# Kernel optimization log

Measured on AMD Instinct MI355X. Metric: run time of the kernel, lower is better.

The kernel has to match this reference:

```python
import jax, jax.numpy as jnp
import numpy as np

BS, N, H, W, C3D, K = 2, 4096, 64, 192, 64, 3


def _leaky(x):
    return jnp.where(x >= 0, x, 0.1 * x)


def setup_inputs() -> dict:
    key = jax.random.key(0)
    ks = jax.random.split(key, 10)
    # uv: pixel coordinates (x in [0,W), y in [0,H)), channel-first [bs,2,N]
    uv = jax.random.uniform(ks[0], (BS, 2, N), dtype=jnp.float32)
    uv = uv * jnp.array([W, H], dtype=jnp.float32)[None, :, None]
    feat_2d = jax.random.normal(ks[1], (BS, 64, H, W), dtype=jnp.float32)
    feat_3d = jax.random.normal(ks[2], (BS, C3D, N), dtype=jnp.float32)
    w1 = jax.random.normal(ks[3], (16, 3), dtype=jnp.float32) * 0.3
    b1 = jax.random.normal(ks[4], (16,), dtype=jnp.float32) * 0.1
    w2 = jax.random.normal(ks[5], (C3D, 16), dtype=jnp.float32) * 0.2
    b2 = jax.random.normal(ks[6], (C3D,), dtype=jnp.float32) * 0.1
    w_out = jax.random.normal(ks[7], (C3D, C3D), dtype=jnp.float32) * 0.1
    b_out = jax.random.normal(ks[8], (C3D,), dtype=jnp.float32) * 0.1
    return {"uv": uv, "feat_2d": feat_2d, "feat_3d": feat_3d,
            "w1": w1, "b1": b1, "w2": w2, "b2": b2,
            "w_out": w_out, "b_out": b_out}


def reference(uv, feat_2d, feat_3d, w1, b1, w2, b2, w_out, b_out):
    bs, _, image_h, image_w = feat_2d.shape
    c3d = feat_3d.shape[1]
    hw = image_h * image_w

    # mesh grid, channel order (x, y), flattened row-major over (h, w): [bs,2,HW]
    ys, xs = jnp.meshgrid(jnp.arange(image_h, dtype=jnp.float32),
                          jnp.arange(image_w, dtype=jnp.float32), indexing='ij')
    grid = jnp.stack([xs.ravel(), ys.ravel()], axis=0)  # [2, HW]
    grid = jnp.broadcast_to(grid[None], (bs, 2, hw))

    # k-NN of uv points for each grid query: squared distances [bs, HW, N]
    d2 = (jnp.sum(grid * grid, axis=1)[:, :, None]
          + jnp.sum(uv * uv, axis=1)[:, None, :]
          - 2.0 * jnp.einsum('bcq,bcn->bqn', grid, uv))
    _, knn_idx = jax.lax.top_k(-d2, K)  # [bs, HW, K]

    # gather uv and feat_3d by neighbor indices: [bs, 2+C, HW, K]
    data = jnp.concatenate([uv, feat_3d], axis=1)
    knn = jax.vmap(lambda d, i: d[:, i])(data, knn_idx)
    knn_uv, knn_feat3d = knn[:, :2], knn[:, 2:]

    knn_offset = knn_uv - grid[..., None]                      # [bs,2,HW,K]
    offset_norm = jnp.linalg.norm(knn_offset, axis=1, keepdims=True)
    score_in = jnp.concatenate([knn_offset, offset_norm], 1)   # [bs,3,HW,K]

    # score net: 1x1 conv (3->16, leaky_relu 0.1) -> 1x1 conv (16->C, sigmoid)
    h1 = _leaky(jnp.einsum('bcqk,oc->boqk', score_in, w1) + b1[None, :, None, None])
    score = jax.nn.sigmoid(jnp.einsum('bcqk,oc->boqk', h1, w2) + b2[None, :, None, None])

    final = jnp.sum(score * knn_feat3d, axis=-1)               # [bs,C,HW]
    final = final.reshape(bs, c3d, image_h, image_w)

    # out conv: 1x1 conv (C->C) + leaky_relu 0.1
    out = _leaky(jnp.einsum('bchw,oc->bohw', final, w_out) + b_out[None, :, None, None])
    return out
```

## Files before the change

kernel.cpp:

```cpp
#include <hip/hip_runtime.h>
#include <math.h>

#define NBS 2
#define NPTS 4096
#define HH 64
#define WW 192
#define HW (HH*WW)
#define NC 64
#define GX 48
#define GY 16
#define NCELL (GX*GY)
#define CSB 1024

#define FBIG 3.0e38f
#define IBIG 0x7FFFFFFF

__global__ __launch_bounds__(256) void k0_prep(
    const float* __restrict__ uv, const float* __restrict__ f3d,
    float* __restrict__ f3dT, float4* __restrict__ binned,
    int* __restrict__ cellStart) {
#pragma clang fp contract(off)
  int bid = blockIdx.x;
  int t = threadIdx.x;
  if (bid < 2) {
    int b = bid;
    __shared__ int hist[NCELL];
    __shared__ int cum[NCELL];
    __shared__ int cur[NCELL];
    for (int c = t; c < NCELL; c += 256) hist[c] = 0;
    __syncthreads();
    const float* u0p = uv + (size_t)b * 2 * NPTS;
    const float* u1p = u0p + NPTS;
    for (int n = t; n < NPTS; n += 256) {
      float u0 = u0p[n], u1 = u1p[n];
      int cxp = min((int)(u0 * 0.25f), GX - 1);
      int cyp = min((int)(u1 * 0.25f), GY - 1);
      atomicAdd(&hist[cyp * GX + cxp], 1);
    }
    __syncthreads();
    if (t < 64) {
      int carry = 0;
#pragma unroll
      for (int ck = 0; ck < NCELL / 64; ++ck) {
        int v = hist[ck * 64 + t];
#pragma unroll
        for (int off = 1; off < 64; off <<= 1) {
          int u = __shfl_up(v, off);
          if (t >= off) v += u;
        }
        cum[ck * 64 + t] = v + carry;
        carry += __shfl(v, 63);
      }
    }
    __syncthreads();
    if (t == 0) cellStart[b * CSB] = 0;
    for (int c = t; c < NCELL; c += 256) {
      cellStart[b * CSB + c + 1] = cum[c];
      cur[c] = cum[c] - hist[c];
    }
    __syncthreads();
    for (int n = t; n < NPTS; n += 256) {
      float u0 = u0p[n], u1 = u1p[n];
      float s0 = u0 * u0;
      float s1 = u1 * u1;
      float uu = s0 + s1;
      int cxp = min((int)(u0 * 0.25f), GX - 1);
      int cyp = min((int)(u1 * 0.25f), GY - 1);
      int pos = atomicAdd(&cur[cyp * GX + cxp], 1);
      binned[(size_t)b * NPTS + pos] =
          make_float4(u0 + u0, u1 + u1, uu, __int_as_float(n));
    }
  } else {
    int bb = bid - 2;
    int b = bb >> 7;
    int half = (bb >> 6) & 1;
    int nt = (bb & 63) << 6;
    __shared__ float tile[32][65];
    int n_in = t & 63;
    int r0 = t >> 6;
    const float* src = f3d + (size_t)b * NC * NPTS + (size_t)half * 32 * NPTS;
#pragma unroll
    for (int r = 0; r < 8; ++r) {
      int c = r0 + (r << 2);
      tile[c][n_in] = src[(size_t)c * NPTS + nt + n_in];
    }
    __syncthreads();
    float* dst = f3dT + ((size_t)b * NPTS + nt) * NC + half * 32;
    int c_out = t & 31;
    int n0 = t >> 5;
#pragma unroll
    for (int r = 0; r < 8; ++r) {
      int n = n0 + (r << 3);
      dst[(size_t)n * NC + c_out] = tile[c_out][n];
    }
  }
}

__global__ __launch_bounds__(256) void k_main(
    const float4* __restrict__ binned, const int* __restrict__ cellStart,
    const float* __restrict__ uv, const float* __restrict__ f3dT,
    const float* __restrict__ w1, const float* __restrict__ b1,
    const float* __restrict__ w2, const float* __restrict__ b2,
    const float* __restrict__ w_out, const float* __restrict__ b_out,
    float* __restrict__ out) {
#pragma clang fp contract(off)
  int t = threadIdx.x;
  int b = blockIdx.y;

  __shared__ int sidx[16][4];
  __shared__ float sh1f[16 * 52];
  __shared__ float fin[16][68];

  {
    int Q = t >> 4;
    int j = t & 15;
    int qi = blockIdx.x * 16 + Q;
    int x = qi % WW, y = qi / WW;
    float xf = (float)x, yf = (float)y;
    float gg = xf * xf + yf * yf;
    int cx = x >> 2, cy = y >> 2;

    const float4* __restrict__ pts = binned + (size_t)b * NPTS;
    const int* __restrict__ cs = cellStart + b * CSB;

    float v0 = FBIG, v1 = FBIG, v2 = FBIG;
    int i0 = IBIG, i1 = IBIG, i2 = IBIG;

    auto ins = [&](float d, int gi) {
      bool dup = (gi == i0) || (gi == i1) || (gi == i2);
      bool lt2 = !dup && ((d < v2) || (d == v2 && gi < i2));
      bool lt1 = !dup && ((d < v1) || (d == v1 && gi < i1));
      bool lt0 = !dup && ((d < v0) || (d == v0 && gi < i0));
      i2 = lt1 ? i1 : (lt2 ? gi : i2);
      v2 = lt1 ? v1 : (lt2 ? d : v2);
      i1 = lt0 ? i0 : (lt1 ? gi : i1);
      v1 = lt0 ? v0 : (lt1 ? d : v1);
      i0 = lt0 ? gi : i0;
      v0 = lt0 ? d : v0;
    };
    auto scanRow = [&](int ry, int cA, int cB) {
      int s = cs[ry * GX + cA];
      int e = cs[ry * GX + cB + 1];
      for (int n = s + j; n < e; n += 16) {
        float4 p = pts[n];
        float d = (gg + p.z) - __builtin_fmaf(yf, p.y, xf * p.x);
        ins(d, __float_as_int(p.w));
      }
    };
    auto mergeAll = [&]() {
#pragma unroll
      for (int m = 1; m <= 8; m <<= 1) {
        float ov0 = __shfl_xor(v0, m), ov1 = __shfl_xor(v1, m),
              ov2 = __shfl_xor(v2, m);
        int oi0 = __shfl_xor(i0, m), oi1 = __shfl_xor(i1, m),
            oi2 = __shfl_xor(i2, m);
        ins(ov0, oi0); ins(ov1, oi1); ins(ov2, oi2);
      }
    };

    int cxL = max(cx - 1, 0), cxH = min(cx + 1, GX - 1);
    int cyL = max(cy - 1, 0), cyH = min(cy + 1, GY - 1);
    for (int ry = cyL; ry <= cyH; ++ry) scanRow(ry, cxL, cxH);
    mergeAll();

    while (true) {
      bool fullDom = (cxL == 0 && cxH == GX - 1 && cyL == 0 && cyH == GY - 1);
      float dL = (cxL > 0) ? (xf - (float)(cxL * 4)) : FBIG;
      float dR = (cxH < GX - 1) ? ((float)((cxH + 1) * 4) - xf) : FBIG;
      float dB = (cyL > 0) ? (yf - (float)(cyL * 4)) : FBIG;
      float dT = (cyH < GY - 1) ? ((float)((cyH + 1) * 4) - yf) : FBIG;
      float dmin = fminf(fminf(dL, dR), fminf(dB, dT));
      if (fullDom || (v2 < dmin * dmin - 1.0f)) break;
      int nxL = max(cxL - 1, 0), nxH = min(cxH + 1, GX - 1);
      int nyL = max(cyL - 1, 0), nyH = min(cyH + 1, GY - 1);
      for (int ry = nyL; ry <= nyH; ++ry) {
        if (ry < cyL || ry > cyH) scanRow(ry, nxL, nxH);
        else {
          if (nxL < cxL) scanRow(ry, nxL, cxL - 1);
          if (nxH > cxH) scanRow(ry, cxH + 1, nxH);
        }
      }
      cxL = nxL; cxH = nxH; cyL = nyL; cyH = nyH;
      mergeAll();
    }

    if (j == 0) { sidx[Q][0] = i0; sidx[Q][1] = i1; sidx[Q][2] = i2; }
  }
  __syncthreads();

  {
    int Q = t >> 4;
    int o = t & 15;
    int qi = blockIdx.x * 16 + Q;
    float xf = (float)(qi % WW);
    float yf = (float)(qi / WW);
    float wa = w1[o * 3 + 0], wb = w1[o * 3 + 1], wc = w1[o * 3 + 2];
    float bo = b1[o];
#pragma unroll
    for (int k = 0; k < 3; ++k) {
      int i = sidx[Q][k];
      float u0 = uv[(size_t)b * 2 * NPTS + i];
      float u1 = uv[(size_t)b * 2 * NPTS + NPTS + i];
      float dx = u0 - xf;
      float dy = u1 - yf;
      float nrm = sqrtf(__builtin_fmaf(dx, dx, dy * dy));
      float h = fmaf(wa, dx, fmaf(wb, dy, fmaf(wc, nrm, bo)));
      sh1f[Q * 52 + k * 16 + o] = (h >= 0.0f) ? h : 0.1f * h;
    }
  }
  __syncthreads();

  {
    int ql = t & 15;
    int cg = t >> 4;
    float h1a[3][16];
    {
      const float4* h4 = (const float4*)(sh1f + ql * 52);
#pragma unroll
      for (int i = 0; i < 12; ++i) {
        float4 v = h4[i];
        int k = i >> 2, oo = (i & 3) * 4;
        h1a[k][oo + 0] = v.x; h1a[k][oo + 1] = v.y;
        h1a[k][oo + 2] = v.z; h1a[k][oo + 3] = v.w;
      }
    }
    int idx[3] = {sidx[ql][0], sidx[ql][1], sidx[ql][2]};
    float4 f0 = *(const float4*)(f3dT + ((size_t)b * NPTS + idx[0]) * NC + cg * 4);
    float4 f1 = *(const float4*)(f3dT + ((size_t)b * NPTS + idx[1]) * NC + cg * 4);
    float4 f2 = *(const float4*)(f3dT + ((size_t)b * NPTS + idx[2]) * NC + cg * 4);
    float fa[4] = {f0.x, f0.y, f0.z, f0.w};
    float fb[4] = {f1.x, f1.y, f1.z, f1.w};
    float fc[4] = {f2.x, f2.y, f2.z, f2.w};
#pragma unroll
    for (int cc = 0; cc < 4; ++cc) {
      int c = cg * 4 + cc;
      float bias = b2[c];
      float s0 = bias, s1 = bias, s2 = bias;
      const float4* w2r = (const float4*)(w2 + c * 16);
#pragma unroll
      for (int o4 = 0; o4 < 4; ++o4) {
        float4 wv = w2r[o4];
        float wvs[4] = {wv.x, wv.y, wv.z, wv.w};
#pragma unroll
        for (int oo = 0; oo < 4; ++oo) {
          int o = o4 * 4 + oo;
          s0 = fmaf(wvs[oo], h1a[0][o], s0);
          s1 = fmaf(wvs[oo], h1a[1][o], s1);
          s2 = fmaf(wvs[oo], h1a[2][o], s2);
        }
      }
      float g0 = 1.0f / (1.0f + __expf(-s0));
      float g1 = 1.0f / (1.0f + __expf(-s1));
      float g2 = 1.0f / (1.0f + __expf(-s2));
      fin[ql][c] = fmaf(g0, fa[cc], fmaf(g1, fb[cc], g2 * fc[cc]));
    }
  }
  __syncthreads();

  {
    int qb = t & 15;
    int cgb = t >> 4;
    int q = blockIdx.x * 16 + qb;
    int o0 = cgb * 4;
    float acc[4];
#pragma unroll
    for (int jj = 0; jj < 4; ++jj) acc[jj] = b_out[o0 + jj];
    const float4* finq = (const float4*)(&fin[qb][0]);
#pragma unroll 4
    for (int c4 = 0; c4 < 16; ++c4) {
      float4 f = finq[c4];
#pragma unroll
      for (int jj = 0; jj < 4; ++jj) {
        float4 wv = *(const float4*)(w_out + (o0 + jj) * 64 + c4 * 4);
        acc[jj] = fmaf(wv.x, f.x,
                  fmaf(wv.y, f.y,
                  fmaf(wv.z, f.z,
                  fmaf(wv.w, f.w, acc[jj]))));
      }
    }
    float* dst = out + ((size_t)(b * 64 + o0)) * HW + q;
#pragma unroll
    for (int jj = 0; jj < 4; ++jj) {
      float v = acc[jj];
      dst[(size_t)jj * HW] = (v >= 0.0f) ? v : 0.1f * v;
    }
  }
}

extern "C" void kernel_launch(void* const* d_in, const int* in_sizes, int n_in,
                              void* d_out, int out_size, void* d_ws, size_t ws_size,
                              hipStream_t stream) {
  const float* uv   = (const float*)d_in[0];
  const float* f3d  = (const float*)d_in[2];
  const float* w1   = (const float*)d_in[3];
  const float* b1   = (const float*)d_in[4];
  const float* w2   = (const float*)d_in[5];
  const float* b2   = (const float*)d_in[6];
  const float* wout = (const float*)d_in[7];
  const float* bout = (const float*)d_in[8];
  float* out = (float*)d_out;

  char* ws = (char*)d_ws;
  float*  f3dT      = (float*)(ws);
  float4* binned    = (float4*)(ws + 2097152);
  int*    cellStart = (int*)(ws + 2228224);

  hipLaunchKernelGGL(k0_prep, dim3(258), dim3(256), 0, stream,
                     uv, f3d, f3dT, binned, cellStart);
  hipLaunchKernelGGL(k_main, dim3(HW / 16, NBS), dim3(256), 0, stream,
                     (const float4*)binned, (const int*)cellStart,
                     uv, f3dT, w1, b1, w2, b2, wout, bout, out);
}
```

Baseline: 48.11 us.

## Fuse knn result into score stages in registers and drop dedup in scan inserts

After the per-query shuffle merge, every lane of the 16-lane group already holds the same top-3, so the score MLP now uses those registers directly. Each lane recomputes all 16 hidden units for its query, and the sidx/sh1f shared buffers and two __syncthreads barriers are removed. The scan-phase insert drops the duplicate check, since each point is visited only once per lane, while the merge keeps it. In exchange, the first-layer work is repeated 16 times per query and register pressure rises.

```diff
diff --git a/kernel.cpp b/kernel.cpp
--- a/kernel.cpp
+++ b/kernel.cpp
@@ -106,27 +106,34 @@
 #pragma clang fp contract(off)
   int t = threadIdx.x;
   int b = blockIdx.y;
-
-  __shared__ int sidx[16][4];
-  __shared__ float sh1f[16 * 52];
+  int Q = t >> 4;
+  int j = t & 15;
+  int qi = blockIdx.x * 16 + Q;
+  int x = qi % WW, y = qi / WW;
+  float xf = (float)x, yf = (float)y;
+  float gg = xf * xf + yf * yf;
+
   __shared__ float fin[16][68];
 
+  float v0 = FBIG, v1 = FBIG, v2 = FBIG;
+  int i0 = IBIG, i1 = IBIG, i2 = IBIG;
   {
-    int Q = t >> 4;
-    int j = t & 15;
-    int qi = blockIdx.x * 16 + Q;
-    int x = qi % WW, y = qi / WW;
-    float xf = (float)x, yf = (float)y;
-    float gg = xf * xf + yf * yf;
     int cx = x >> 2, cy = y >> 2;
-
     const float4* __restrict__ pts = binned + (size_t)b * NPTS;
     const int* __restrict__ cs = cellStart + b * CSB;
 
-    float v0 = FBIG, v1 = FBIG, v2 = FBIG;
-    int i0 = IBIG, i1 = IBIG, i2 = IBIG;
-
-    auto ins = [&](float d, int gi) {
+    auto insS = [&](float d, int gi) {
+      bool lt2 = (d < v2) || (d == v2 && gi < i2);
+      bool lt1 = (d < v1) || (d == v1 && gi < i1);
+      bool lt0 = (d < v0) || (d == v0 && gi < i0);
+      i2 = lt1 ? i1 : (lt2 ? gi : i2);
+      v2 = lt1 ? v1 : (lt2 ? d : v2);
+      i1 = lt0 ? i0 : (lt1 ? gi : i1);
+      v1 = lt0 ? v0 : (lt1 ? d : v1);
+      i0 = lt0 ? gi : i0;
+      v0 = lt0 ? d : v0;
+    };
+    auto insM = [&](float d, int gi) {
       bool dup = (gi == i0) || (gi == i1) || (gi == i2);
       bool lt2 = !dup && ((d < v2) || (d == v2 && gi < i2));
       bool lt1 = !dup && ((d < v1) || (d == v1 && gi < i1));
@@ -144,7 +151,7 @@
       for (int n = s + j; n < e; n += 16) {
         float4 p = pts[n];
         float d = (gg + p.z) - __builtin_fmaf(yf, p.y, xf * p.x);
-        ins(d, __float_as_int(p.w));
+        insS(d, __float_as_int(p.w));
       }
     };
     auto mergeAll = [&]() {
@@ -154,7 +161,7 @@
               ov2 = __shfl_xor(v2, m);
         int oi0 = __shfl_xor(i0, m), oi1 = __shfl_xor(i1, m),
             oi2 = __shfl_xor(i2, m);
-        ins(ov0, oi0); ins(ov1, oi1); ins(ov2, oi2);
+        insM(ov0, oi0); insM(ov1, oi1); insM(ov2, oi2);
       }
     };
 
@@ -183,57 +190,38 @@
       cxL = nxL; cxH = nxH; cyL = nyL; cyH = nyH;
       mergeAll();
     }
-
-    if (j == 0) { sidx[Q][0] = i0; sidx[Q][1] = i1; sidx[Q][2] = i2; }
   }
-  __syncthreads();
 
   {
-    int Q = t >> 4;
-    int o = t & 15;
-    int qi = blockIdx.x * 16 + Q;
-    float xf = (float)(qi % WW);
-    float yf = (float)(qi / WW);
-    float wa = w1[o * 3 + 0], wb = w1[o * 3 + 1], wc = w1[o * 3 + 2];
-    float bo = b1[o];
+    int idx[3] = {i0, i1, i2};
+    float h1a[3][16];
 #pragma unroll
     for (int k = 0; k < 3; ++k) {
-      int i = sidx[Q][k];
+      int i = idx[k];
       float u0 = uv[(size_t)b * 2 * NPTS + i];
       float u1 = uv[(size_t)b * 2 * NPTS + NPTS + i];
       float dx = u0 - xf;
       float dy = u1 - yf;
       float nrm = sqrtf(__builtin_fmaf(dx, dx, dy * dy));
-      float h = fmaf(wa, dx, fmaf(wb, dy, fmaf(wc, nrm, bo)));
-      sh1f[Q * 52 + k * 16 + o] = (h >= 0.0f) ? h : 0.1f * h;
-    }
-  }
-  __syncthreads();
-
-  {
-    int ql = t & 15;
-    int cg = t >> 4;
-    float h1a[3][16];
-    {
-      const float4* h4 = (const float4*)(sh1f + ql * 52);
-#pragma unroll
-      for (int i = 0; i < 12; ++i) {
-        float4 v = h4[i];
-        int k = i >> 2, oo = (i & 3) * 4;
-        h1a[k][oo + 0] = v.x; h1a[k][oo + 1] = v.y;
-        h1a[k][oo + 2] = v.z; h1a[k][oo + 3] = v.w;
-      }
-    }
-    int idx[3] = {sidx[ql][0], sidx[ql][1], sidx[ql][2]};
-    float4 f0 = *(const float4*)(f3dT + ((size_t)b * NPTS + idx[0]) * NC + cg * 4);
-    float4 f1 = *(const float4*)(f3dT + ((size_t)b * NPTS + idx[1]) * NC + cg * 4);
-    float4 f2 = *(const float4*)(f3dT + ((size_t)b * NPTS + idx[2]) * NC + cg * 4);
+#pragma unroll
+      for (int o = 0; o < 16; ++o) {
+        float h = fmaf(w1[o * 3 + 0], dx,
+                 fmaf(w1[o * 3 + 1], dy,
+                 fmaf(w1[o * 3 + 2], nrm, b1[o])));
+        h1a[k][o] = (h >= 0.0f) ? h : 0.1f * h;
+      }
+    }
+
+    float4 f0 = *(const float4*)(f3dT + ((size_t)b * NPTS + idx[0]) * NC + j * 4);
+    float4 f1 = *(const float4*)(f3dT + ((size_t)b * NPTS + idx[1]) * NC + j * 4);
+    float4 f2 = *(const float4*)(f3dT + ((size_t)b * NPTS + idx[2]) * NC + j * 4);
     float fa[4] = {f0.x, f0.y, f0.z, f0.w};
     float fb[4] = {f1.x, f1.y, f1.z, f1.w};
     float fc[4] = {f2.x, f2.y, f2.z, f2.w};
+    float res[4];
 #pragma unroll
     for (int cc = 0; cc < 4; ++cc) {
-      int c = cg * 4 + cc;
+      int c = j * 4 + cc;
       float bias = b2[c];
       float s0 = bias, s1 = bias, s2 = bias;
       const float4* w2r = (const float4*)(w2 + c * 16);
@@ -252,8 +240,9 @@
       float g0 = 1.0f / (1.0f + __expf(-s0));
       float g1 = 1.0f / (1.0f + __expf(-s1));
       float g2 = 1.0f / (1.0f + __expf(-s2));
-      fin[ql][c] = fmaf(g0, fa[cc], fmaf(g1, fb[cc], g2 * fc[cc]));
-    }
+      res[cc] = fmaf(g0, fa[cc], fmaf(g1, fb[cc], g2 * fc[cc]));
+    }
+    *(float4*)(&fin[Q][j * 4]) = make_float4(res[0], res[1], res[2], res[3]);
   }
   __syncthreads();
 
```

Result: slower. 52.45 us (+9.0%).
